# Optimization experiments

Measured on AMD Instinct MI355X. Metric: run time of the kernel, lower is better.

The kernel has to match this reference:

```python
import jax, jax.numpy as jnp
import numpy as np

EMBED_DIM = 1024
NUM_HEADS = 16
HEAD_DIM = EMBED_DIM // NUM_HEADS
LN_EPS = 1e-5


def setup_inputs() -> dict:
    key = jax.random.key(0)
    ks = jax.random.split(key, 7)
    B, N, D = 4, 2048, EMBED_DIM
    s = 1.0 / np.sqrt(D)  # ~kaiming-uniform scale for Linear weights
    return {
        "inputs": jax.random.normal(ks[0], (B, N, D), dtype=jnp.float32),
        "W_q": jax.random.uniform(ks[1], (D, D), jnp.float32, -s, s),
        "W_k": jax.random.uniform(ks[2], (D, D), jnp.float32, -s, s),
        "W_v": jax.random.uniform(ks[3], (D, D), jnp.float32, -s, s),
        "W_o": jax.random.uniform(ks[4], (D, D), jnp.float32, -s, s),
        "ln_gamma": jnp.ones((D,), jnp.float32),
        "ln_beta": jnp.zeros((D,), jnp.float32),
    }


def reference(inputs, W_q, W_k, W_v, W_o, ln_gamma, ln_beta):
    x = inputs
    B, N, D = x.shape
    H, Hd = NUM_HEADS, HEAD_DIM
    # torch nn.Linear computes x @ W.T; W_* stored as (out, in)
    q = (x @ W_q.T).reshape(B, N, H, Hd).transpose(0, 2, 1, 3)  # [B,H,N,Hd]
    k = (x @ W_k.T).reshape(B, N, H, Hd).transpose(0, 2, 1, 3)
    v = (x @ W_v.T).reshape(B, N, H, Hd).transpose(0, 2, 1, 3)
    scores = jnp.einsum("bhqd,bhkd->bhqk", q, k) / jnp.sqrt(jnp.float32(Hd))
    attn = jax.nn.softmax(scores, axis=-1)  # dropout p=0 -> identity
    out = jnp.einsum("bhqk,bhkd->bhqd", attn, v)
    out = out.transpose(0, 2, 1, 3).reshape(B, N, D)
    out = out @ W_o.T
    # residual + LayerNorm
    y = out + x
    mu = jnp.mean(y, axis=-1, keepdims=True)
    var = jnp.mean(jnp.square(y - mu), axis=-1, keepdims=True)
    y = (y - mu) * jax.lax.rsqrt(var + LN_EPS)
    return y * ln_gamma + ln_beta
```

## Files before the change

### kernel.cpp

```cpp
#include <hip/hip_runtime.h>
#include <hip/hip_bf16.h>
#include <stdint.h>

typedef __attribute__((ext_vector_type(8))) short bf16x8;
typedef __attribute__((ext_vector_type(4))) float f32x4;

#define GLOBAL_AS __attribute__((address_space(1)))
#define LDS_AS    __attribute__((address_space(3)))

__device__ __forceinline__ void load_lds16(const void* g, void* l) {
  __builtin_amdgcn_global_load_lds((const GLOBAL_AS void*)g, (LDS_AS void*)l, 16, 0, 0);
}

__device__ __forceinline__ short f2bfn(float f) {
  __hip_bfloat16 h = __float2bfloat16(f);
  return __builtin_bit_cast(short, h);
}

__global__ __launch_bounds__(256) void cvt_bf16(const float* __restrict__ in,
                                                short* __restrict__ out, int n) {
  int i = (blockIdx.x * 256 + threadIdx.x) * 8;
  if (i >= n) return;
  float4 a = *(const float4*)(in + i);
  float4 b = *(const float4*)(in + i + 4);
  bf16x8 o;
  o[0] = f2bfn(a.x); o[1] = f2bfn(a.y); o[2] = f2bfn(a.z); o[3] = f2bfn(a.w);
  o[4] = f2bfn(b.x); o[5] = f2bfn(b.y); o[6] = f2bfn(b.z); o[7] = f2bfn(b.w);
  *(bf16x8*)(out + i) = o;
}

__global__ __launch_bounds__(256) void cvt_w(const float* __restrict__ q,
                                             const float* __restrict__ k,
                                             const float* __restrict__ v,
                                             const float* __restrict__ o,
                                             short* __restrict__ Wb,
                                             short* __restrict__ Wob) {
  const int sel = blockIdx.x >> 9;
  const int inner = blockIdx.x & 511;
  const int i = (inner * 256 + threadIdx.x) * 8;
  const float* src = sel == 0 ? q : sel == 1 ? k : sel == 2 ? v : o;
  short* dst = sel == 0 ? Wb : sel == 1 ? Wb + 1024 * 1024
             : sel == 2 ? Wb + 2 * 1024 * 1024 : Wob;
  float4 a = *(const float4*)(src + i);
  float4 b = *(const float4*)(src + i + 4);
  bf16x8 ov;
  ov[0] = f2bfn(a.x); ov[1] = f2bfn(a.y); ov[2] = f2bfn(a.z); ov[3] = f2bfn(a.w);
  ov[4] = f2bfn(b.x); ov[5] = f2bfn(b.y); ov[6] = f2bfn(b.z); ov[7] = f2bfn(b.w);
  *(bf16x8*)(dst + i) = ov;
}

template<int OUT_BF16>
__global__ __launch_bounds__(256) void gemm_bt(const short* __restrict__ A,
                                               const short* __restrict__ B,
                                               void* __restrict__ Cp,
                                               int M, int N, int K) {
  __shared__ short As[128 * 64];
  __shared__ short Bs[128 * 64];
  const int t = threadIdx.x, l = t & 63, w = t >> 6;
  const int g = l >> 4, li = l & 15;
  const int wr = w >> 1, wc = w & 1;
  const int bid = blockIdx.x;
  const int bm = (bid & 7) * 8 + ((bid >> 3) & 7);
  const int bn = bid >> 6;
  const int sw = li & 7;
  f32x4 acc[4][4] = {};
  const size_t arow0 = (size_t)(bm * 128) * K;
  const size_t brow0 = (size_t)(bn * 128) * K;
  for (int k0 = 0; k0 < K; k0 += 64) {
    __syncthreads();
#pragma unroll
    for (int it = 0; it < 4; ++it) {
      int e = it * 2048 + t * 8;
      int r = e >> 6;
      int cs = (e >> 3) & 7;
      int cg = cs ^ (r & 7);
      load_lds16(A + arow0 + (size_t)r * K + (k0 + cg * 8), &As[e]);
      load_lds16(B + brow0 + (size_t)r * K + (k0 + cg * 8), &Bs[e]);
    }
    __syncthreads();
#pragma unroll
    for (int kk = 0; kk < 2; ++kk) {
      bf16x8 af[4], bfr[4];
#pragma unroll
      for (int m = 0; m < 4; ++m)
        af[m] = *(const bf16x8*)&As[(wr * 64 + m * 16 + li) * 64 + (((kk * 4 + g) ^ sw) * 8)];
#pragma unroll
      for (int n = 0; n < 4; ++n)
        bfr[n] = *(const bf16x8*)&Bs[(wc * 64 + n * 16 + li) * 64 + (((kk * 4 + g) ^ sw) * 8)];
#pragma unroll
      for (int m = 0; m < 4; ++m)
#pragma unroll
        for (int n = 0; n < 4; ++n)
          acc[m][n] = __builtin_amdgcn_mfma_f32_16x16x32_bf16(af[m], bfr[n], acc[m][n], 0, 0, 0);
    }
  }
#pragma unroll
  for (int m = 0; m < 4; ++m)
#pragma unroll
    for (int n = 0; n < 4; ++n)
#pragma unroll
      for (int r = 0; r < 4; ++r) {
        int row = bm * 128 + wr * 64 + m * 16 + g * 4 + r;
        int col = bn * 128 + wc * 64 + n * 16 + li;
        if (OUT_BF16)
          ((short*)Cp)[(size_t)row * N + col] = f2bfn(acc[m][n][r]);
        else
          ((float*)Cp)[(size_t)row * N + col] = acc[m][n][r];
      }
}

__global__ __launch_bounds__(256) void transpose_v(const short* __restrict__ qkv,
                                                   short* __restrict__ VT) {
  const int kt = blockIdx.x;
  const int bh = blockIdx.y;
  const int b = bh >> 4, h = bh & 15;
  __shared__ short T[64][72];
  const int t = threadIdx.x;
  const size_t src = (size_t)b * 2048 * 3072 + 2048 + (size_t)h * 64;
#pragma unroll
  for (int i = 0; i < 2; ++i) {
    int k = i * 32 + (t >> 3);
    int d0 = (t & 7) * 8;
    bf16x8 v = *(const bf16x8*)(qkv + src + (size_t)(kt * 64 + k) * 3072 + d0);
#pragma unroll
    for (int j = 0; j < 8; ++j) T[d0 + j][k] = v[j];
  }
  __syncthreads();
#pragma unroll
  for (int i = 0; i < 2; ++i) {
    int d = i * 32 + (t >> 3);
    int k0 = (t & 7) * 8;
    bf16x8 v = *(const bf16x8*)&T[d][k0];
    *(bf16x8*)(VT + ((size_t)bh * 64 + d) * 2048 + kt * 64 + k0) = v;
  }
}

__global__ __launch_bounds__(256, 3) void attn_fwd(const short* __restrict__ qkv,
                                                   const short* __restrict__ VT,
                                                   short* __restrict__ obuf) {
  const int f0 = blockIdx.x;
  const int work = (f0 & 7) * 128 + (f0 >> 3);
  const int qt = work & 15;
  const int bh = work >> 4;
  const int b = bh >> 4, h = bh & 15;
  const int t = threadIdx.x, w = t >> 6, l = t & 63;
  const int g = l >> 4, li = l & 15;

  __shared__ short Ks[2][64 * 64];
  __shared__ short Vts[2][64 * 64];
  __shared__ short Ps[4][2][16 * 64];

  const size_t base = (size_t)b * 2048 * 3072 + (size_t)h * 64;
  const short* Vsrc = VT + (size_t)bh * 64 * 2048;

  bf16x8 qf[2][2];
  {
    const float QSC = 0.125f * 1.44269504088896341f;
#pragma unroll
    for (int qh = 0; qh < 2; ++qh) {
      const short* qp = qkv + base + (size_t)(qt * 128 + w * 32 + qh * 16 + li) * 3072;
#pragma unroll
      for (int c = 0; c < 2; ++c) {
        bf16x8 v = *(const bf16x8*)(qp + c * 32 + g * 8);
#pragma unroll
        for (int i = 0; i < 8; ++i) {
          float f = __uint_as_float(((unsigned)(unsigned short)v[i]) << 16);
          v[i] = f2bfn(f * QSC);
        }
        qf[qh][c] = v;
      }
    }
  }

  bf16x8 ones;
#pragma unroll
  for (int i = 0; i < 8; ++i) ones[i] = (short)0x3F80;

  float m_[2] = {-1e30f, -1e30f};
  f32x4 o_[2][4], lacc[2];
#pragma unroll
  for (int qh = 0; qh < 2; ++qh) {
#pragma unroll
    for (int dj = 0; dj < 4; ++dj) o_[qh][dj] = (f32x4){0.f, 0.f, 0.f, 0.f};
    lacc[qh] = (f32x4){0.f, 0.f, 0.f, 0.f};
  }

  const int sw = li & 7;

#define STAGE(buf, kt_)                                                          \
  {                                                                              \
    _Pragma("unroll")                                                            \
    for (int it = 0; it < 2; ++it) {                                             \
      int e = it * 2048 + t * 8;                                                 \
      int r = e >> 6;                                                            \
      int cs = (e >> 3) & 7;                                                     \
      int cg = cs ^ (r & 7);                                                     \
      load_lds16(qkv + base + 1024 + (size_t)((kt_) * 64 + r) * 3072 + cg * 8,   \
                 &Ks[buf][e]);                                                   \
      load_lds16(Vsrc + (size_t)r * 2048 + (kt_) * 64 + cg * 8, &Vts[buf][e]);   \
    }                                                                            \
  }

  STAGE(0, 0);
  asm volatile("s_waitcnt vmcnt(0)" ::: "memory");
  __syncthreads();

  for (int kt = 0; kt < 32; ++kt) {
    const int cur = kt & 1;
    if (kt + 1 < 32) STAGE(cur ^ 1, kt + 1);

    f32x4 s_[2][4];
#pragma unroll
    for (int qh = 0; qh < 2; ++qh)
#pragma unroll
      for (int j = 0; j < 4; ++j) s_[qh][j] = (f32x4){0.f, 0.f, 0.f, 0.f};
    __builtin_amdgcn_s_setprio(1);
#pragma unroll
    for (int c = 0; c < 2; ++c)
#pragma unroll
      for (int j = 0; j < 4; ++j) {
        bf16x8 kf = *(const bf16x8*)&Ks[cur][(j * 16 + li) * 64 + (((c * 4 + g) ^ sw) * 8)];
        s_[0][j] = __builtin_amdgcn_mfma_f32_16x16x32_bf16(kf, qf[0][c], s_[0][j], 0, 0, 0);
        s_[1][j] = __builtin_amdgcn_mfma_f32_16x16x32_bf16(kf, qf[1][c], s_[1][j], 0, 0, 0);
      }
    __builtin_amdgcn_s_setprio(0);

    float mt[2];
#pragma unroll
    for (int qh = 0; qh < 2; ++qh) {
      float a0 = fmaxf(fmaxf(s_[qh][0][0], s_[qh][0][1]), s_[qh][0][2]);
      float a1 = fmaxf(fmaxf(s_[qh][0][3], s_[qh][1][0]), s_[qh][1][1]);
      float a2 = fmaxf(fmaxf(s_[qh][1][2], s_[qh][1][3]), s_[qh][2][0]);
      float a3 = fmaxf(fmaxf(s_[qh][2][1], s_[qh][2][2]), s_[qh][2][3]);
      float a4 = fmaxf(fmaxf(s_[qh][3][0], s_[qh][3][1]), s_[qh][3][2]);
      float b0 = fmaxf(fmaxf(a0, a1), a2);
      float b1 = fmaxf(fmaxf(a3, a4), s_[qh][3][3]);
      float m0 = fmaxf(b0, b1);
      m0 = fmaxf(m0, __shfl_xor(m0, 16));
      m0 = fmaxf(m0, __shfl_xor(m0, 32));
      mt[qh] = m0;
    }

    bool ok = (mt[0] <= m_[0] + 8.f) && (mt[1] <= m_[1] + 8.f);
    if (!__all(ok)) {
#pragma unroll
      for (int qh = 0; qh < 2; ++qh) {
        float mn = fmaxf(m_[qh], mt[qh]);
        float al = exp2f(m_[qh] - mn);
        m_[qh] = mn;
#pragma unroll
        for (int r = 0; r < 4; ++r) {
          float alr = __shfl(al, (l & 48) | (g * 4 + r));
#pragma unroll
          for (int dj = 0; dj < 4; ++dj) o_[qh][dj][r] *= alr;
          lacc[qh][r] *= alr;
        }
      }
    }

#pragma unroll
    for (int qh = 0; qh < 2; ++qh) {
#pragma unroll
      for (int j = 0; j < 4; ++j) {
        float p0 = exp2f(s_[qh][j][0] - m_[qh]);
        float p1 = exp2f(s_[qh][j][1] - m_[qh]);
        float p2 = exp2f(s_[qh][j][2] - m_[qh]);
        float p3 = exp2f(s_[qh][j][3] - m_[qh]);
        unsigned u0, u1;
        asm("v_cvt_pk_bf16_f32 %0, %1, %2" : "=v"(u0) : "v"(p0), "v"(p1));
        asm("v_cvt_pk_bf16_f32 %0, %1, %2" : "=v"(u1) : "v"(p2), "v"(p3));
        uint2 pk2; pk2.x = u0; pk2.y = u1;
        int pos = (j * 16 + g * 4) ^ (sw << 3);
        *(uint2*)&Ps[w][qh][li * 64 + pos] = pk2;
      }
    }
    asm volatile("s_waitcnt lgkmcnt(0)" ::: "memory");

    __builtin_amdgcn_s_setprio(1);
#pragma unroll
    for (int c = 0; c < 2; ++c) {
      bf16x8 vb[4];
#pragma unroll
      for (int dj = 0; dj < 4; ++dj)
        vb[dj] = *(const bf16x8*)&Vts[cur][(dj * 16 + li) * 64 + (((c * 4 + g) ^ sw) * 8)];
#pragma unroll
      for (int qh = 0; qh < 2; ++qh) {
        bf16x8 pa = *(const bf16x8*)&Ps[w][qh][li * 64 + (((c * 4 + g) ^ sw) * 8)];
        lacc[qh] = __builtin_amdgcn_mfma_f32_16x16x32_bf16(pa, ones, lacc[qh], 0, 0, 0);
#pragma unroll
        for (int dj = 0; dj < 4; ++dj)
          o_[qh][dj] = __builtin_amdgcn_mfma_f32_16x16x32_bf16(pa, vb[dj], o_[qh][dj], 0, 0, 0);
      }
    }
    __builtin_amdgcn_s_setprio(0);

    asm volatile("s_waitcnt vmcnt(0)" ::: "memory");
    __syncthreads();
  }

#pragma unroll
  for (int qh = 0; qh < 2; ++qh)
#pragma unroll
    for (int r = 0; r < 4; ++r) {
      float ilr = 1.f / lacc[qh][r];
      int row = b * 2048 + qt * 128 + w * 32 + qh * 16 + g * 4 + r;
#pragma unroll
      for (int dj = 0; dj < 4; ++dj) {
        int col = h * 64 + dj * 16 + li;
        obuf[(size_t)row * 1024 + col] = f2bfn(o_[qh][dj][r] * ilr);
      }
    }
#undef STAGE
}

__global__ __launch_bounds__(256) void resid_ln(const float* __restrict__ U,
                                                const float* __restrict__ x,
                                                const float* __restrict__ gamma,
                                                const float* __restrict__ beta,
                                                float* __restrict__ out) {
  const int row = blockIdx.x;
  const int t = threadIdx.x, w = t >> 6, l = t & 63;
  const float4 uu = *(const float4*)(U + (size_t)row * 1024 + t * 4);
  const float4 xx = *(const float4*)(x + (size_t)row * 1024 + t * 4);
  float y[4] = {uu.x + xx.x, uu.y + xx.y, uu.z + xx.z, uu.w + xx.w};
  float s = (y[0] + y[1]) + (y[2] + y[3]);
#pragma unroll
  for (int d = 1; d < 64; d <<= 1) s += __shfl_xor(s, d);
  __shared__ float red[4];
  if (l == 0) red[w] = s;
  __syncthreads();
  s = red[0] + red[1] + red[2] + red[3];
  const float mu = s * (1.f / 1024.f);
  float vs = 0.f;
#pragma unroll
  for (int i = 0; i < 4; ++i) { float d0 = y[i] - mu; vs += d0 * d0; }
#pragma unroll
  for (int d = 1; d < 64; d <<= 1) vs += __shfl_xor(vs, d);
  __syncthreads();
  if (l == 0) red[w] = vs;
  __syncthreads();
  vs = red[0] + red[1] + red[2] + red[3];
  const float rstd = rsqrtf(vs * (1.f / 1024.f) + 1e-5f);
  const float4 gg = *(const float4*)(gamma + t * 4);
  const float4 bb = *(const float4*)(beta + t * 4);
  float4 oo;
  oo.x = (y[0] - mu) * rstd * gg.x + bb.x;
  oo.y = (y[1] - mu) * rstd * gg.y + bb.y;
  oo.z = (y[2] - mu) * rstd * gg.z + bb.z;
  oo.w = (y[3] - mu) * rstd * gg.w + bb.w;
  *(float4*)(out + (size_t)row * 1024 + t * 4) = oo;
}

extern "C" void kernel_launch(void* const* d_in, const int* in_sizes, int n_in,
                              void* d_out, int out_size, void* d_ws, size_t ws_size,
                              hipStream_t stream) {
  const float* x     = (const float*)d_in[0];
  const float* W_q   = (const float*)d_in[1];
  const float* W_k   = (const float*)d_in[2];
  const float* W_v   = (const float*)d_in[3];
  const float* W_o   = (const float*)d_in[4];
  const float* gamma = (const float*)d_in[5];
  const float* beta  = (const float*)d_in[6];
  float* out = (float*)d_out;

  char* ws = (char*)d_ws;
  short* xb   = (short*)ws;  ws += (size_t)8192 * 1024 * 2;
  short* Wb   = (short*)ws;  ws += (size_t)3072 * 1024 * 2;
  short* Wob  = (short*)ws;  ws += (size_t)1024 * 1024 * 2;
  short* qkv  = (short*)ws;  ws += (size_t)8192 * 3072 * 2;
  short* obuf = (short*)ws;  ws += (size_t)8192 * 1024 * 2;
  float* U    = (float*)ws;  ws += (size_t)8192 * 1024 * 4;
  short* VT   = (short*)U;

  cvt_bf16<<<4096, 256, 0, stream>>>(x, xb, 8192 * 1024);
  cvt_w<<<2048, 256, 0, stream>>>(W_q, W_k, W_v, W_o, Wb, Wob);

  gemm_bt<1><<<1536, 256, 0, stream>>>(xb, Wb, qkv, 8192, 3072, 1024);
  transpose_v<<<dim3(32, 64), 256, 0, stream>>>(qkv, VT);
  attn_fwd<<<1024, 256, 0, stream>>>(qkv, VT, obuf);
  gemm_bt<0><<<512, 256, 0, stream>>>(obuf, Wob, U, 8192, 1024, 1024);
  resid_ln<<<8192, 256, 0, stream>>>(U, x, gamma, beta, out);
}
```

Measured before the change: 238.9 us.

## Compute V transposed directly via swapped GEMM and enlarge attention blocks to 512 threads

The V projection is now a separate GEMM computing W_v·x^T, so the output is written straight into the per-head transposed VT layout. This removes the standalone transpose kernel and its extra pass over V. The QKV GEMM now produces only Q and K into the strided qkv buffer. The attention kernel goes to 8 waves per block with 256 query rows, so each staged K/V tile is shared by twice as many queries and the load loop shrinks to one iteration per thread. The VT GEMM writes scattered 2-byte values with stride 2048, which may give poor store coalescing, and the larger blocks change occupancy.

```diff
diff --git a/kernel.cpp b/kernel.cpp
--- a/kernel.cpp
+++ b/kernel.cpp
@@ -49,19 +49,20 @@
   *(bf16x8*)(dst + i) = ov;
 }
 
-template<int OUT_BF16>
+template<int MODE>
 __global__ __launch_bounds__(256) void gemm_bt(const short* __restrict__ A,
                                                const short* __restrict__ B,
                                                void* __restrict__ Cp,
-                                               int M, int N, int K) {
+                                               int M, int N, int K, int ldc) {
   __shared__ short As[128 * 64];
   __shared__ short Bs[128 * 64];
   const int t = threadIdx.x, l = t & 63, w = t >> 6;
   const int g = l >> 4, li = l & 15;
   const int wr = w >> 1, wc = w & 1;
   const int bid = blockIdx.x;
-  const int bm = (bid & 7) * 8 + ((bid >> 3) & 7);
-  const int bn = bid >> 6;
+  int bm, bn;
+  if (MODE == 2) { bm = bid & 7; bn = bid >> 3; }
+  else { bm = (bid & 7) * 8 + ((bid >> 3) & 7); bn = bid >> 6; }
   const int sw = li & 7;
   f32x4 acc[4][4] = {};
   const size_t arow0 = (size_t)(bm * 128) * K;
@@ -102,53 +103,30 @@
       for (int r = 0; r < 4; ++r) {
         int row = bm * 128 + wr * 64 + m * 16 + g * 4 + r;
         int col = bn * 128 + wc * 64 + n * 16 + li;
-        if (OUT_BF16)
-          ((short*)Cp)[(size_t)row * N + col] = f2bfn(acc[m][n][r]);
+        if (MODE == 0)
+          ((float*)Cp)[(size_t)row * ldc + col] = acc[m][n][r];
+        else if (MODE == 1)
+          ((short*)Cp)[(size_t)row * ldc + col] = f2bfn(acc[m][n][r]);
         else
-          ((float*)Cp)[(size_t)row * N + col] = acc[m][n][r];
-      }
-}
-
-__global__ __launch_bounds__(256) void transpose_v(const short* __restrict__ qkv,
-                                                   short* __restrict__ VT) {
-  const int kt = blockIdx.x;
-  const int bh = blockIdx.y;
-  const int b = bh >> 4, h = bh & 15;
-  __shared__ short T[64][72];
-  const int t = threadIdx.x;
-  const size_t src = (size_t)b * 2048 * 3072 + 2048 + (size_t)h * 64;
-#pragma unroll
-  for (int i = 0; i < 2; ++i) {
-    int k = i * 32 + (t >> 3);
-    int d0 = (t & 7) * 8;
-    bf16x8 v = *(const bf16x8*)(qkv + src + (size_t)(kt * 64 + k) * 3072 + d0);
-#pragma unroll
-    for (int j = 0; j < 8; ++j) T[d0 + j][k] = v[j];
-  }
-  __syncthreads();
-#pragma unroll
-  for (int i = 0; i < 2; ++i) {
-    int d = i * 32 + (t >> 3);
-    int k0 = (t & 7) * 8;
-    bf16x8 v = *(const bf16x8*)&T[d][k0];
-    *(bf16x8*)(VT + ((size_t)bh * 64 + d) * 2048 + kt * 64 + k0) = v;
-  }
-}
-
-__global__ __launch_bounds__(256, 3) void attn_fwd(const short* __restrict__ qkv,
+          ((short*)Cp)[(size_t)(col >> 11) * (1024 * 2048) + (size_t)row * 2048 +
+                       (col & 2047)] = f2bfn(acc[m][n][r]);
+      }
+}
+
+__global__ __launch_bounds__(512, 4) void attn_fwd(const short* __restrict__ qkv,
                                                    const short* __restrict__ VT,
                                                    short* __restrict__ obuf) {
   const int f0 = blockIdx.x;
-  const int work = (f0 & 7) * 128 + (f0 >> 3);
-  const int qt = work & 15;
-  const int bh = work >> 4;
+  const int work = (f0 & 7) * 64 + (f0 >> 3);
+  const int qt = work & 7;
+  const int bh = work >> 3;
   const int b = bh >> 4, h = bh & 15;
   const int t = threadIdx.x, w = t >> 6, l = t & 63;
   const int g = l >> 4, li = l & 15;
 
   __shared__ short Ks[2][64 * 64];
   __shared__ short Vts[2][64 * 64];
-  __shared__ short Ps[4][2][16 * 64];
+  __shared__ short Ps[8][2][16 * 64];
 
   const size_t base = (size_t)b * 2048 * 3072 + (size_t)h * 64;
   const short* Vsrc = VT + (size_t)bh * 64 * 2048;
@@ -158,7 +136,7 @@
     const float QSC = 0.125f * 1.44269504088896341f;
 #pragma unroll
     for (int qh = 0; qh < 2; ++qh) {
-      const short* qp = qkv + base + (size_t)(qt * 128 + w * 32 + qh * 16 + li) * 3072;
+      const short* qp = qkv + base + (size_t)(qt * 256 + w * 32 + qh * 16 + li) * 3072;
 #pragma unroll
       for (int c = 0; c < 2; ++c) {
         bf16x8 v = *(const bf16x8*)(qp + c * 32 + g * 8);
@@ -189,16 +167,13 @@
 
 #define STAGE(buf, kt_)                                                          \
   {                                                                              \
-    _Pragma("unroll")                                                            \
-    for (int it = 0; it < 2; ++it) {                                             \
-      int e = it * 2048 + t * 8;                                                 \
-      int r = e >> 6;                                                            \
-      int cs = (e >> 3) & 7;                                                     \
-      int cg = cs ^ (r & 7);                                                     \
-      load_lds16(qkv + base + 1024 + (size_t)((kt_) * 64 + r) * 3072 + cg * 8,   \
-                 &Ks[buf][e]);                                                   \
-      load_lds16(Vsrc + (size_t)r * 2048 + (kt_) * 64 + cg * 8, &Vts[buf][e]);   \
-    }                                                                            \
+    int e = t * 8;                                                               \
+    int r = e >> 6;                                                              \
+    int cs = (e >> 3) & 7;                                                       \
+    int cg = cs ^ (r & 7);                                                       \
+    load_lds16(qkv + base + 1024 + (size_t)((kt_) * 64 + r) * 3072 + cg * 8,     \
+               &Ks[buf][e]);                                                     \
+    load_lds16(Vsrc + (size_t)r * 2048 + (kt_) * 64 + cg * 8, &Vts[buf][e]);     \
   }
 
   STAGE(0, 0);
@@ -303,7 +278,7 @@
 #pragma unroll
     for (int r = 0; r < 4; ++r) {
       float ilr = 1.f / lacc[qh][r];
-      int row = b * 2048 + qt * 128 + w * 32 + qh * 16 + g * 4 + r;
+      int row = b * 2048 + qt * 256 + w * 32 + qh * 16 + g * 4 + r;
 #pragma unroll
       for (int dj = 0; dj < 4; ++dj) {
         int col = h * 64 + dj * 16 + li;
@@ -375,9 +350,9 @@
   cvt_bf16<<<4096, 256, 0, stream>>>(x, xb, 8192 * 1024);
   cvt_w<<<2048, 256, 0, stream>>>(W_q, W_k, W_v, W_o, Wb, Wob);
 
-  gemm_bt<1><<<1536, 256, 0, stream>>>(xb, Wb, qkv, 8192, 3072, 1024);
-  transpose_v<<<dim3(32, 64), 256, 0, stream>>>(qkv, VT);
-  attn_fwd<<<1024, 256, 0, stream>>>(qkv, VT, obuf);
-  gemm_bt<0><<<512, 256, 0, stream>>>(obuf, Wob, U, 8192, 1024, 1024);
+  gemm_bt<1><<<1024, 256, 0, stream>>>(xb, Wb, qkv, 8192, 2048, 1024, 3072);
+  gemm_bt<2><<<512, 256, 0, stream>>>(Wb + 2 * 1024 * 1024, xb, VT, 1024, 8192, 1024, 0);
+  attn_fwd<<<512, 512, 0, stream>>>(qkv, VT, obuf);
+  gemm_bt<0><<<512, 256, 0, stream>>>(obuf, Wob, U, 8192, 1024, 1024, 1024);
   resid_ln<<<8192, 256, 0, stream>>>(U, x, gamma, beta, out);
 }
```

After: 233.5 us. -2.2%, faster.
